# Optimization experiments

Measured on AMD Instinct MI355X. Metric: run time of the kernel, lower is better.

Reference implementation:

```python
import jax, jax.numpy as jnp
import numpy as np

GENES = 20000   # input gene nodes (depth 0)
LEVEL = 10000   # nodes per subsequent depth level
STEPS = 7       # depth propagation steps
DEG = 16        # in-degree per dst node
N = GENES + STEPS * LEVEL          # 90000 total nodes
EPS = LEVEL * DEG                  # 160000 edges per step
E = STEPS * EPS                    # 1120000 total edges
B = 256
C = 2


def setup_inputs() -> dict:
    key = jax.random.key(0)
    k0, k1, k2 = jax.random.split(key, 3)
    X = jax.random.normal(k0, (B, GENES), jnp.float32)
    gene_map = jnp.arange(GENES, dtype=jnp.int32)

    rng = np.random.default_rng(0)
    src_list, dstu_list = [], []
    for k in range(STEPS):
        lo = 0 if k == 0 else GENES + (k - 1) * LEVEL
        hi = GENES if k == 0 else lo + LEVEL
        src_list.append(rng.integers(lo, hi, size=EPS))
        dstu_list.append(np.arange(GENES + k * LEVEL, GENES + (k + 1) * LEVEL))
    src = jnp.asarray(np.stack(src_list), dtype=jnp.int32)          # [STEPS, EPS]
    dst_unique = jnp.asarray(np.stack(dstu_list), dtype=jnp.int32)  # [STEPS, LEVEL]
    dst_pos = jnp.tile(jnp.repeat(jnp.arange(LEVEL, dtype=jnp.int32), DEG)[None, :], (STEPS, 1))
    eid = jnp.arange(E, dtype=jnp.int32).reshape(STEPS, EPS)
    root_ids = dst_unique[-1]

    edge_weight = jax.random.normal(k1, (E,), jnp.float32) * 0.01
    node_bias = jnp.zeros((N,), jnp.float32)
    head_W = jax.random.normal(k2, (LEVEL, C), jnp.float32) * (1.0 / np.sqrt(LEVEL))
    head_b = jnp.zeros((C,), jnp.float32)

    return dict(X=X, edge_weight=edge_weight, node_bias=node_bias,
                head_W=head_W, head_b=head_b, gene_map=gene_map,
                src=src, dst_pos=dst_pos, dst_unique=dst_unique,
                eid=eid, root_ids=root_ids)


def reference(X, edge_weight, node_bias, head_W, head_b,
              gene_map, src, dst_pos, dst_unique, eid, root_ids):
    # dropout is identity (eval mode / p=0)
    b = X.shape[0]
    h = jnp.zeros((b, N), X.dtype).at[:, gene_map].set(X)
    for k in range(src.shape[0]):  # fixed small number of depth steps
        w = edge_weight[eid[k]]                                   # [EPS]
        msg = h[:, src[k]] * w[None, :]                           # gather + scale [B, EPS]
        agg = jnp.zeros((b, dst_unique.shape[1]), h.dtype).at[:, dst_pos[k]].add(msg)
        h_dst = jnp.tanh(agg + node_bias[dst_unique[k]][None, :])  # [B, LEVEL]
        h = h.at[:, dst_unique[k]].set(h_dst)
    roots = h[:, root_ids]                                        # [B, LEVEL]
    return roots @ head_W + head_b
```

## Files before the change

### kernel.cpp

```cpp
#include <hip/hip_runtime.h>
#include <math.h>

#define GENES 20000
#define LEVEL 10000
#define STEPS 7
#define DEG   16
#define EPSZ  (LEVEL * DEG)
#define CCOLS 32
#define NCHUNK 8
#define DBLK  313
#define NGT   625
#define MSTRIDE 18
#define SCOLS 8
#define DPG   1250

typedef unsigned short bf8 __attribute__((ext_vector_type(8)));

__device__ inline float bf2f(unsigned short u) {
    union { unsigned u; float f; } c; c.u = ((unsigned)u) << 16; return c.f;
}
__device__ inline unsigned short f2bf(float x) {
    union { float f; unsigned u; } c; c.f = x;
    return (unsigned short)((c.u + 0x7fffu + ((c.u >> 16) & 1u)) >> 16);
}

__global__ __launch_bounds__(256) void transpose_k(const float* __restrict__ X,
                                                   const int*   __restrict__ gene_map,
                                                   unsigned short* __restrict__ XT) {
    __shared__ float tile[32][33];
    const int chunk = blockIdx.x;
    const int l4  = threadIdx.x & 7;
    const int r8  = threadIdx.x >> 3;
    const int lo  = threadIdx.x & 31;
    const int gr8 = threadIdx.x >> 5;
    unsigned short* XTp = XT + (size_t)chunk * GENES * CCOLS;
    for (int i = 0; i < 4; ++i) {
        const int gt = blockIdx.y * 4 + i;
        if (gt >= NGT) break;
        const int g0 = gt * 32;
        if (i) __syncthreads();
        const float4 xv = *reinterpret_cast<const float4*>(
            X + (size_t)(chunk * CCOLS + r8) * GENES + g0 + l4 * 4);
        tile[r8][l4 * 4 + 0] = xv.x;
        tile[r8][l4 * 4 + 1] = xv.y;
        tile[r8][l4 * 4 + 2] = xv.z;
        tile[r8][l4 * 4 + 3] = xv.w;
        __syncthreads();
#pragma unroll
        for (int jj = 0; jj < 4; ++jj) {
            const int gr   = gr8 + jj * 8;
            const int node = gene_map[g0 + gr];
            XTp[(size_t)node * CCOLS + lo] = f2bf(tile[lo][gr]);
        }
    }
}

__global__ __launch_bounds__(256) void step1_k(const unsigned short* __restrict__ hprev,
                                               unsigned short*       __restrict__ hcur,
                                               const int*   __restrict__ src_k,
                                               const float* __restrict__ w_k,
                                               const float* __restrict__ node_bias,
                                               const int*   __restrict__ dstu_k) {
    const int bid   = blockIdx.x;
    const int chunk = bid & 7;
    const int cb    = bid >> 3;
    const int tid   = threadIdx.x;

    __shared__ int   s_src[32 * MSTRIDE];
    __shared__ float s_w  [32 * MSTRIDE];

    if (tid < 128) {
        const int m4 = cb * 128 + tid;
        if (m4 < EPSZ / 4) {
            const int4 sv = reinterpret_cast<const int4*>(src_k)[m4];
            const int j = tid >> 2, i = (tid & 3) * 4;
            *reinterpret_cast<int4*>(&s_src[j * MSTRIDE + i]) = sv;
        }
    } else {
        const int t  = tid - 128;
        const int m4 = cb * 128 + t;
        if (m4 < EPSZ / 4) {
            const float4 wv = reinterpret_cast<const float4*>(w_k)[m4];
            const int j = t >> 2, i = (t & 3) * 4;
            *reinterpret_cast<float4*>(&s_w[j * MSTRIDE + i]) = wv;
        }
    }
    __syncthreads();

    const int wave = tid >> 6, lane = tid & 63;
    const int c2 = lane & 3;
    const int eh = (lane >> 2) & 1;
    const int q  = lane >> 3;
    const int j  = wave * 8 + q;
    const int dest = cb * 32 + j;
    const int c8 = c2 * 8;

    if (dest < LEVEL) {
        const unsigned short* prev = hprev + (size_t)chunk * GENES * CCOLS;

        const int mb = j * MSTRIDE + eh * 8;
        const int4   sA = *reinterpret_cast<const int4*>  (&s_src[mb]);
        const int4   sB = *reinterpret_cast<const int4*>  (&s_src[mb + 4]);
        const float4 wA = *reinterpret_cast<const float4*>(&s_w  [mb]);
        const float4 wB = *reinterpret_cast<const float4*>(&s_w  [mb + 4]);

#define GL(sv) (*reinterpret_cast<const bf8*>(prev + (size_t)(sv) * CCOLS + c8))
        const bf8 v0 = GL(sA.x);
        const bf8 v1 = GL(sA.y);
        const bf8 v2 = GL(sA.z);
        const bf8 v3 = GL(sA.w);
        const bf8 v4 = GL(sB.x);
        const bf8 v5 = GL(sB.y);
        const bf8 v6 = GL(sB.z);
        const bf8 v7 = GL(sB.w);
#undef GL
        float a0 = 0.f, a1 = 0.f, a2 = 0.f, a3 = 0.f, a4 = 0.f, a5 = 0.f, a6 = 0.f, a7 = 0.f;
#define FMA8(v, wv) { a0 = fmaf(bf2f((v)[0]), (wv), a0); a1 = fmaf(bf2f((v)[1]), (wv), a1);  \
                      a2 = fmaf(bf2f((v)[2]), (wv), a2); a3 = fmaf(bf2f((v)[3]), (wv), a3);  \
                      a4 = fmaf(bf2f((v)[4]), (wv), a4); a5 = fmaf(bf2f((v)[5]), (wv), a5);  \
                      a6 = fmaf(bf2f((v)[6]), (wv), a6); a7 = fmaf(bf2f((v)[7]), (wv), a7); }
        FMA8(v0, wA.x) FMA8(v1, wA.y) FMA8(v2, wA.z) FMA8(v3, wA.w)
        FMA8(v4, wB.x) FMA8(v5, wB.y) FMA8(v6, wB.z) FMA8(v7, wB.w)
#undef FMA8
        a0 += __shfl_xor(a0, 4); a1 += __shfl_xor(a1, 4);
        a2 += __shfl_xor(a2, 4); a3 += __shfl_xor(a3, 4);
        a4 += __shfl_xor(a4, 4); a5 += __shfl_xor(a5, 4);
        a6 += __shfl_xor(a6, 4); a7 += __shfl_xor(a7, 4);

        if (eh == 0) {
            const float bz = node_bias[dstu_k[dest]];
            bf8 o;
            o[0] = f2bf(tanhf(a0 + bz));
            o[1] = f2bf(tanhf(a1 + bz));
            o[2] = f2bf(tanhf(a2 + bz));
            o[3] = f2bf(tanhf(a3 + bz));
            o[4] = f2bf(tanhf(a4 + bz));
            o[5] = f2bf(tanhf(a5 + bz));
            o[6] = f2bf(tanhf(a6 + bz));
            o[7] = f2bf(tanhf(a7 + bz));
            *reinterpret_cast<bf8*>(hcur + ((size_t)(chunk * 4 + c2) * LEVEL + dest) * SCOLS) = o;
        }
    }
}

__global__ __launch_bounds__(1024) void sstep_k(
        const unsigned short* __restrict__ hprev,
        unsigned short*       __restrict__ hcur,
        const int*   __restrict__ src_k,
        const float* __restrict__ w_k,
        const float* __restrict__ node_bias,
        const int*   __restrict__ dstu_k,
        int src_base) {
    __shared__ unsigned short slice[LEVEL * SCOLS];
    const int bid = blockIdx.x;
    const int cc  = (bid & 7) * 4 + ((bid >> 3) & 3);
    const int g   = bid >> 5;
    const int tid = threadIdx.x;

    const int d0 = g * DPG + tid;
    const int be0 = d0 * DEG;
    const int4   sA = *reinterpret_cast<const int4*>  (src_k + be0);
    const int4   sB = *reinterpret_cast<const int4*>  (src_k + be0 + 4);
    const int4   sC = *reinterpret_cast<const int4*>  (src_k + be0 + 8);
    const int4   sD = *reinterpret_cast<const int4*>  (src_k + be0 + 12);
    const float4 wA = *reinterpret_cast<const float4*>(w_k + be0);
    const float4 wB = *reinterpret_cast<const float4*>(w_k + be0 + 4);
    const float4 wC = *reinterpret_cast<const float4*>(w_k + be0 + 8);
    const float4 wD = *reinterpret_cast<const float4*>(w_k + be0 + 12);

    const unsigned short* pc = hprev + (size_t)cc * LEVEL * SCOLS;
#pragma unroll
    for (int i = 0; i < 10; ++i) {
        const int row = i * 1024 + tid;
        if (row < LEVEL)
            *reinterpret_cast<bf8*>(&slice[row * SCOLS]) =
                *reinterpret_cast<const bf8*>(pc + (size_t)row * SCOLS);
    }
    __syncthreads();

    unsigned short* oc = hcur + (size_t)cc * LEVEL * SCOLS;

#define ACC(sv, wv) { const int row = (sv) - src_base;                                      \
    const bf8 v = *reinterpret_cast<const bf8*>(&slice[row * SCOLS]);                       \
    a0 = fmaf(bf2f(v[0]), (wv), a0); a1 = fmaf(bf2f(v[1]), (wv), a1);                       \
    a2 = fmaf(bf2f(v[2]), (wv), a2); a3 = fmaf(bf2f(v[3]), (wv), a3);                       \
    a4 = fmaf(bf2f(v[4]), (wv), a4); a5 = fmaf(bf2f(v[5]), (wv), a5);                       \
    a6 = fmaf(bf2f(v[6]), (wv), a6); a7 = fmaf(bf2f(v[7]), (wv), a7); }

    {
        float a0 = 0.f, a1 = 0.f, a2 = 0.f, a3 = 0.f, a4 = 0.f, a5 = 0.f, a6 = 0.f, a7 = 0.f;
        ACC(sA.x, wA.x) ACC(sA.y, wA.y) ACC(sA.z, wA.z) ACC(sA.w, wA.w)
        ACC(sB.x, wB.x) ACC(sB.y, wB.y) ACC(sB.z, wB.z) ACC(sB.w, wB.w)
        ACC(sC.x, wC.x) ACC(sC.y, wC.y) ACC(sC.z, wC.z) ACC(sC.w, wC.w)
        ACC(sD.x, wD.x) ACC(sD.y, wD.y) ACC(sD.z, wD.z) ACC(sD.w, wD.w)
        const float bz = node_bias[dstu_k[d0]];
        bf8 o;
        o[0] = f2bf(tanhf(a0 + bz));
        o[1] = f2bf(tanhf(a1 + bz));
        o[2] = f2bf(tanhf(a2 + bz));
        o[3] = f2bf(tanhf(a3 + bz));
        o[4] = f2bf(tanhf(a4 + bz));
        o[5] = f2bf(tanhf(a5 + bz));
        o[6] = f2bf(tanhf(a6 + bz));
        o[7] = f2bf(tanhf(a7 + bz));
        *reinterpret_cast<bf8*>(oc + (size_t)d0 * SCOLS) = o;
    }

    if (tid < DPG - 1024) {
        const int d1 = g * DPG + 1024 + tid;
        const int be1 = d1 * DEG;
        const int4   tA = *reinterpret_cast<const int4*>  (src_k + be1);
        const int4   tB = *reinterpret_cast<const int4*>  (src_k + be1 + 4);
        const int4   tC = *reinterpret_cast<const int4*>  (src_k + be1 + 8);
        const int4   tD = *reinterpret_cast<const int4*>  (src_k + be1 + 12);
        const float4 uA = *reinterpret_cast<const float4*>(w_k + be1);
        const float4 uB = *reinterpret_cast<const float4*>(w_k + be1 + 4);
        const float4 uC = *reinterpret_cast<const float4*>(w_k + be1 + 8);
        const float4 uD = *reinterpret_cast<const float4*>(w_k + be1 + 12);
        float a0 = 0.f, a1 = 0.f, a2 = 0.f, a3 = 0.f, a4 = 0.f, a5 = 0.f, a6 = 0.f, a7 = 0.f;
        ACC(tA.x, uA.x) ACC(tA.y, uA.y) ACC(tA.z, uA.z) ACC(tA.w, uA.w)
        ACC(tB.x, uB.x) ACC(tB.y, uB.y) ACC(tB.z, uB.z) ACC(tB.w, uB.w)
        ACC(tC.x, uC.x) ACC(tC.y, uC.y) ACC(tC.z, uC.z) ACC(tC.w, uC.w)
        ACC(tD.x, uD.x) ACC(tD.y, uD.y) ACC(tD.z, uD.z) ACC(tD.w, uD.w)
        const float bz = node_bias[dstu_k[d1]];
        bf8 o;
        o[0] = f2bf(tanhf(a0 + bz));
        o[1] = f2bf(tanhf(a1 + bz));
        o[2] = f2bf(tanhf(a2 + bz));
        o[3] = f2bf(tanhf(a3 + bz));
        o[4] = f2bf(tanhf(a4 + bz));
        o[5] = f2bf(tanhf(a5 + bz));
        o[6] = f2bf(tanhf(a6 + bz));
        o[7] = f2bf(tanhf(a7 + bz));
        *reinterpret_cast<bf8*>(oc + (size_t)d1 * SCOLS) = o;
    }
#undef ACC
}

__global__ __launch_bounds__(1024) void sstep7_k(
        const unsigned short* __restrict__ hprev,
        const int*   __restrict__ src_k,
        const float* __restrict__ w_k,
        const float* __restrict__ node_bias,
        const int*   __restrict__ dstu_k,
        const float* __restrict__ head_W,
        float*       __restrict__ part,
        int src_base) {
    __shared__ unsigned short slice[LEVEL * SCOLS];
    __shared__ float red[16][16];
    const int bid = blockIdx.x;
    const int cc  = (bid & 7) * 4 + ((bid >> 3) & 3);
    const int g   = bid >> 5;
    const int tid = threadIdx.x;

    const int d0 = g * DPG + tid;
    const int be0 = d0 * DEG;
    const int4   sA = *reinterpret_cast<const int4*>  (src_k + be0);
    const int4   sB = *reinterpret_cast<const int4*>  (src_k + be0 + 4);
    const int4   sC = *reinterpret_cast<const int4*>  (src_k + be0 + 8);
    const int4   sD = *reinterpret_cast<const int4*>  (src_k + be0 + 12);
    const float4 wA = *reinterpret_cast<const float4*>(w_k + be0);
    const float4 wB = *reinterpret_cast<const float4*>(w_k + be0 + 4);
    const float4 wC = *reinterpret_cast<const float4*>(w_k + be0 + 8);
    const float4 wD = *reinterpret_cast<const float4*>(w_k + be0 + 12);

    const unsigned short* pc = hprev + (size_t)cc * LEVEL * SCOLS;
#pragma unroll
    for (int i = 0; i < 10; ++i) {
        const int row = i * 1024 + tid;
        if (row < LEVEL)
            *reinterpret_cast<bf8*>(&slice[row * SCOLS]) =
                *reinterpret_cast<const bf8*>(pc + (size_t)row * SCOLS);
    }
    __syncthreads();

    float h[16];
#pragma unroll
    for (int v = 0; v < 16; ++v) h[v] = 0.f;

#define ACC(sv, wv) { const int row = (sv) - src_base;                                      \
    const bf8 v = *reinterpret_cast<const bf8*>(&slice[row * SCOLS]);                       \
    a0 = fmaf(bf2f(v[0]), (wv), a0); a1 = fmaf(bf2f(v[1]), (wv), a1);                       \
    a2 = fmaf(bf2f(v[2]), (wv), a2); a3 = fmaf(bf2f(v[3]), (wv), a3);                       \
    a4 = fmaf(bf2f(v[4]), (wv), a4); a5 = fmaf(bf2f(v[5]), (wv), a5);                       \
    a6 = fmaf(bf2f(v[6]), (wv), a6); a7 = fmaf(bf2f(v[7]), (wv), a7); }
#define HEADU(d) {                                                                           \
        const float bz = node_bias[dstu_k[d]];                                               \
        const float o0 = tanhf(a0 + bz), o1 = tanhf(a1 + bz);                                \
        const float o2 = tanhf(a2 + bz), o3 = tanhf(a3 + bz);                                \
        const float o4 = tanhf(a4 + bz), o5 = tanhf(a5 + bz);                                \
        const float o6 = tanhf(a6 + bz), o7 = tanhf(a7 + bz);                                \
        const float2 wv = *reinterpret_cast<const float2*>(head_W + (size_t)(d) * 2);        \
        h[0]  = fmaf(o0, wv.x, h[0]);  h[1]  = fmaf(o0, wv.y, h[1]);                         \
        h[2]  = fmaf(o1, wv.x, h[2]);  h[3]  = fmaf(o1, wv.y, h[3]);                         \
        h[4]  = fmaf(o2, wv.x, h[4]);  h[5]  = fmaf(o2, wv.y, h[5]);                         \
        h[6]  = fmaf(o3, wv.x, h[6]);  h[7]  = fmaf(o3, wv.y, h[7]);                         \
        h[8]  = fmaf(o4, wv.x, h[8]);  h[9]  = fmaf(o4, wv.y, h[9]);                         \
        h[10] = fmaf(o5, wv.x, h[10]); h[11] = fmaf(o5, wv.y, h[11]);                        \
        h[12] = fmaf(o6, wv.x, h[12]); h[13] = fmaf(o6, wv.y, h[13]);                        \
        h[14] = fmaf(o7, wv.x, h[14]); h[15] = fmaf(o7, wv.y, h[15]); }

    {
        float a0 = 0.f, a1 = 0.f, a2 = 0.f, a3 = 0.f, a4 = 0.f, a5 = 0.f, a6 = 0.f, a7 = 0.f;
        ACC(sA.x, wA.x) ACC(sA.y, wA.y) ACC(sA.z, wA.z) ACC(sA.w, wA.w)
        ACC(sB.x, wB.x) ACC(sB.y, wB.y) ACC(sB.z, wB.z) ACC(sB.w, wB.w)
        ACC(sC.x, wC.x) ACC(sC.y, wC.y) ACC(sC.z, wC.z) ACC(sC.w, wC.w)
        ACC(sD.x, wD.x) ACC(sD.y, wD.y) ACC(sD.z, wD.z) ACC(sD.w, wD.w)
        HEADU(d0)
    }
    if (tid < DPG - 1024) {
        const int d1 = g * DPG + 1024 + tid;
        const int be1 = d1 * DEG;
        const int4   tA = *reinterpret_cast<const int4*>  (src_k + be1);
        const int4   tB = *reinterpret_cast<const int4*>  (src_k + be1 + 4);
        const int4   tC = *reinterpret_cast<const int4*>  (src_k + be1 + 8);
        const int4   tD = *reinterpret_cast<const int4*>  (src_k + be1 + 12);
        const float4 uA = *reinterpret_cast<const float4*>(w_k + be1);
        const float4 uB = *reinterpret_cast<const float4*>(w_k + be1 + 4);
        const float4 uC = *reinterpret_cast<const float4*>(w_k + be1 + 8);
        const float4 uD = *reinterpret_cast<const float4*>(w_k + be1 + 12);
        float a0 = 0.f, a1 = 0.f, a2 = 0.f, a3 = 0.f, a4 = 0.f, a5 = 0.f, a6 = 0.f, a7 = 0.f;
        ACC(tA.x, uA.x) ACC(tA.y, uA.y) ACC(tA.z, uA.z) ACC(tA.w, uA.w)
        ACC(tB.x, uB.x) ACC(tB.y, uB.y) ACC(tB.z, uB.z) ACC(tB.w, uB.w)
        ACC(tC.x, uC.x) ACC(tC.y, uC.y) ACC(tC.z, uC.z) ACC(tC.w, uC.w)
        ACC(tD.x, uD.x) ACC(tD.y, uD.y) ACC(tD.z, uD.z) ACC(tD.w, uD.w)
        HEADU(d1)
    }
#undef HEADU
#undef ACC

    const int wave = tid >> 6, lane = tid & 63;
#pragma unroll
    for (int m = 1; m < 64; m <<= 1) {
#pragma unroll
        for (int v = 0; v < 16; ++v) h[v] += __shfl_xor(h[v], m);
    }
    if (lane == 0) {
#pragma unroll
        for (int v = 0; v < 16; ++v) red[wave][v] = h[v];
    }
    __syncthreads();
    if (tid < 16) {
        float s = 0.f;
#pragma unroll
        for (int w = 0; w < 16; ++w) s += red[w][tid];
        part[((size_t)cc * 8 + g) * 16 + tid] = s;
    }
}

__global__ __launch_bounds__(512) void head_final_k(const float* __restrict__ part,
                                                    const float* __restrict__ head_b,
                                                    float*       __restrict__ out) {
    const int tid = threadIdx.x;
    const int cc = tid >> 4, v = tid & 15;
    float acc = head_b[v & 1];
#pragma unroll
    for (int g = 0; g < 8; ++g)
        acc += part[((size_t)cc * 8 + g) * 16 + v];
    const int b = (cc >> 2) * 32 + (cc & 3) * 8 + (v >> 1);
    out[b * 2 + (v & 1)] = acc;
}

extern "C" void kernel_launch(void* const* d_in, const int* in_sizes, int n_in,
                              void* d_out, int out_size, void* d_ws, size_t ws_size,
                              hipStream_t stream) {
    const float* X           = (const float*)d_in[0];
    const float* edge_weight = (const float*)d_in[1];
    const float* node_bias   = (const float*)d_in[2];
    const float* head_W      = (const float*)d_in[3];
    const float* head_b      = (const float*)d_in[4];
    const int*   gene_map    = (const int*)  d_in[5];
    const int*   src         = (const int*)  d_in[6];
    const int*   dst_unique  = (const int*)  d_in[8];
    float* out = (float*)d_out;

    char* ws = (char*)d_ws;
    unsigned short* XT   = (unsigned short*)(ws);
    unsigned short* lvlA = (unsigned short*)(ws + 10240000);
    unsigned short* lvlB = (unsigned short*)(ws + 15360000);
    float*          part = (float*)         (ws + 20480000);

    transpose_k<<<dim3(NCHUNK, 157), 256, 0, stream>>>(X, gene_map, XT);

    step1_k<<<DBLK * NCHUNK, 256, 0, stream>>>(XT, lvlA, src, edge_weight,
                                               node_bias, dst_unique);

    unsigned short* bufs[2] = {lvlA, lvlB};
    for (int k = 1; k <= 5; ++k) {
        sstep_k<<<256, 1024, 0, stream>>>(bufs[(k - 1) & 1], bufs[k & 1],
                                          src + (size_t)k * EPSZ,
                                          edge_weight + (size_t)k * EPSZ,
                                          node_bias,
                                          dst_unique + (size_t)k * LEVEL,
                                          GENES + (k - 1) * LEVEL);
    }

    sstep7_k<<<256, 1024, 0, stream>>>(bufs[1],
                                       src + (size_t)6 * EPSZ,
                                       edge_weight + (size_t)6 * EPSZ,
                                       node_bias,
                                       dst_unique + (size_t)6 * LEVEL,
                                       head_W, part,
                                       GENES + 5 * LEVEL);
    head_final_k<<<1, 512, 0, stream>>>(part, head_b, out);
    (void)in_sizes; (void)n_in; (void)out_size; (void)ws_size;
}
```

Baseline: 79.22 us.

## Fuse depth steps 2-7 and head into one persistent kernel with per-chunk counters

Replaces the six per-step launches plus the final head-reduction kernel with one persistent kernel of 256 blocks. Blocks that share a column chunk synchronise through atomic counters in global memory, and each level is written to its own buffer. The weight and index loads for the next step are issued before the wait, so they overlap it. The aim is to remove launch gaps and the tail of each kernel, at the cost of spin-waiting. The design also relies on all 256 blocks being co-resident, and it adds a memset launch.

Result: slower. 138.4 us (+74.7%).

```diff
diff --git a/kernel.cpp b/kernel.cpp
--- a/kernel.cpp
+++ b/kernel.cpp
@@ -3,7 +3,6 @@
 
 #define GENES 20000
 #define LEVEL 10000
-#define STEPS 7
 #define DEG   16
 #define EPSZ  (LEVEL * DEG)
 #define CCOLS 32
@@ -13,6 +12,7 @@
 #define MSTRIDE 18
 #define SCOLS 8
 #define DPG   1250
+#define LVLSZ ((size_t)32 * LEVEL * SCOLS)
 
 typedef unsigned short bf8 __attribute__((ext_vector_type(8)));
 
@@ -143,149 +143,36 @@
     }
 }
 
-__global__ __launch_bounds__(1024) void sstep_k(
-        const unsigned short* __restrict__ hprev,
-        unsigned short*       __restrict__ hcur,
-        const int*   __restrict__ src_k,
-        const float* __restrict__ w_k,
+__global__ __launch_bounds__(1024, 1) void fused_k(
+        unsigned short* lvl,
+        const int*   __restrict__ src,
+        const float* __restrict__ ew,
         const float* __restrict__ node_bias,
-        const int*   __restrict__ dstu_k,
-        int src_base) {
-    __shared__ unsigned short slice[LEVEL * SCOLS];
-    const int bid = blockIdx.x;
-    const int cc  = (bid & 7) * 4 + ((bid >> 3) & 3);
-    const int g   = bid >> 5;
-    const int tid = threadIdx.x;
-
-    const int d0 = g * DPG + tid;
-    const int be0 = d0 * DEG;
-    const int4   sA = *reinterpret_cast<const int4*>  (src_k + be0);
-    const int4   sB = *reinterpret_cast<const int4*>  (src_k + be0 + 4);
-    const int4   sC = *reinterpret_cast<const int4*>  (src_k + be0 + 8);
-    const int4   sD = *reinterpret_cast<const int4*>  (src_k + be0 + 12);
-    const float4 wA = *reinterpret_cast<const float4*>(w_k + be0);
-    const float4 wB = *reinterpret_cast<const float4*>(w_k + be0 + 4);
-    const float4 wC = *reinterpret_cast<const float4*>(w_k + be0 + 8);
-    const float4 wD = *reinterpret_cast<const float4*>(w_k + be0 + 12);
-
-    const unsigned short* pc = hprev + (size_t)cc * LEVEL * SCOLS;
-#pragma unroll
-    for (int i = 0; i < 10; ++i) {
-        const int row = i * 1024 + tid;
-        if (row < LEVEL)
-            *reinterpret_cast<bf8*>(&slice[row * SCOLS]) =
-                *reinterpret_cast<const bf8*>(pc + (size_t)row * SCOLS);
-    }
-    __syncthreads();
-
-    unsigned short* oc = hcur + (size_t)cc * LEVEL * SCOLS;
-
-#define ACC(sv, wv) { const int row = (sv) - src_base;                                      \
-    const bf8 v = *reinterpret_cast<const bf8*>(&slice[row * SCOLS]);                       \
-    a0 = fmaf(bf2f(v[0]), (wv), a0); a1 = fmaf(bf2f(v[1]), (wv), a1);                       \
-    a2 = fmaf(bf2f(v[2]), (wv), a2); a3 = fmaf(bf2f(v[3]), (wv), a3);                       \
-    a4 = fmaf(bf2f(v[4]), (wv), a4); a5 = fmaf(bf2f(v[5]), (wv), a5);                       \
-    a6 = fmaf(bf2f(v[6]), (wv), a6); a7 = fmaf(bf2f(v[7]), (wv), a7); }
-
-    {
-        float a0 = 0.f, a1 = 0.f, a2 = 0.f, a3 = 0.f, a4 = 0.f, a5 = 0.f, a6 = 0.f, a7 = 0.f;
-        ACC(sA.x, wA.x) ACC(sA.y, wA.y) ACC(sA.z, wA.z) ACC(sA.w, wA.w)
-        ACC(sB.x, wB.x) ACC(sB.y, wB.y) ACC(sB.z, wB.z) ACC(sB.w, wB.w)
-        ACC(sC.x, wC.x) ACC(sC.y, wC.y) ACC(sC.z, wC.z) ACC(sC.w, wC.w)
-        ACC(sD.x, wD.x) ACC(sD.y, wD.y) ACC(sD.z, wD.z) ACC(sD.w, wD.w)
-        const float bz = node_bias[dstu_k[d0]];
-        bf8 o;
-        o[0] = f2bf(tanhf(a0 + bz));
-        o[1] = f2bf(tanhf(a1 + bz));
-        o[2] = f2bf(tanhf(a2 + bz));
-        o[3] = f2bf(tanhf(a3 + bz));
-        o[4] = f2bf(tanhf(a4 + bz));
-        o[5] = f2bf(tanhf(a5 + bz));
-        o[6] = f2bf(tanhf(a6 + bz));
-        o[7] = f2bf(tanhf(a7 + bz));
-        *reinterpret_cast<bf8*>(oc + (size_t)d0 * SCOLS) = o;
-    }
-
-    if (tid < DPG - 1024) {
-        const int d1 = g * DPG + 1024 + tid;
-        const int be1 = d1 * DEG;
-        const int4   tA = *reinterpret_cast<const int4*>  (src_k + be1);
-        const int4   tB = *reinterpret_cast<const int4*>  (src_k + be1 + 4);
-        const int4   tC = *reinterpret_cast<const int4*>  (src_k + be1 + 8);
-        const int4   tD = *reinterpret_cast<const int4*>  (src_k + be1 + 12);
-        const float4 uA = *reinterpret_cast<const float4*>(w_k + be1);
-        const float4 uB = *reinterpret_cast<const float4*>(w_k + be1 + 4);
-        const float4 uC = *reinterpret_cast<const float4*>(w_k + be1 + 8);
-        const float4 uD = *reinterpret_cast<const float4*>(w_k + be1 + 12);
-        float a0 = 0.f, a1 = 0.f, a2 = 0.f, a3 = 0.f, a4 = 0.f, a5 = 0.f, a6 = 0.f, a7 = 0.f;
-        ACC(tA.x, uA.x) ACC(tA.y, uA.y) ACC(tA.z, uA.z) ACC(tA.w, uA.w)
-        ACC(tB.x, uB.x) ACC(tB.y, uB.y) ACC(tB.z, uB.z) ACC(tB.w, uB.w)
-        ACC(tC.x, uC.x) ACC(tC.y, uC.y) ACC(tC.z, uC.z) ACC(tC.w, uC.w)
-        ACC(tD.x, uD.x) ACC(tD.y, uD.y) ACC(tD.z, uD.z) ACC(tD.w, uD.w)
-        const float bz = node_bias[dstu_k[d1]];
-        bf8 o;
-        o[0] = f2bf(tanhf(a0 + bz));
-        o[1] = f2bf(tanhf(a1 + bz));
-        o[2] = f2bf(tanhf(a2 + bz));
-        o[3] = f2bf(tanhf(a3 + bz));
-        o[4] = f2bf(tanhf(a4 + bz));
-        o[5] = f2bf(tanhf(a5 + bz));
-        o[6] = f2bf(tanhf(a6 + bz));
-        o[7] = f2bf(tanhf(a7 + bz));
-        *reinterpret_cast<bf8*>(oc + (size_t)d1 * SCOLS) = o;
-    }
-#undef ACC
-}
-
-__global__ __launch_bounds__(1024) void sstep7_k(
-        const unsigned short* __restrict__ hprev,
-        const int*   __restrict__ src_k,
-        const float* __restrict__ w_k,
-        const float* __restrict__ node_bias,
-        const int*   __restrict__ dstu_k,
+        const int*   __restrict__ dst_unique,
         const float* __restrict__ head_W,
-        float*       __restrict__ part,
-        int src_base) {
+        const float* __restrict__ head_b,
+        float* __restrict__ part,
+        int*   __restrict__ cnt,
+        float* __restrict__ out) {
     __shared__ unsigned short slice[LEVEL * SCOLS];
     __shared__ float red[16][16];
     const int bid = blockIdx.x;
     const int cc  = (bid & 7) * 4 + ((bid >> 3) & 3);
     const int g   = bid >> 5;
     const int tid = threadIdx.x;
-
-    const int d0 = g * DPG + tid;
+    int* cc_cnt = cnt + cc * 16;
+
+    const int d0  = g * DPG + tid;
     const int be0 = d0 * DEG;
-    const int4   sA = *reinterpret_cast<const int4*>  (src_k + be0);
-    const int4   sB = *reinterpret_cast<const int4*>  (src_k + be0 + 4);
-    const int4   sC = *reinterpret_cast<const int4*>  (src_k + be0 + 8);
-    const int4   sD = *reinterpret_cast<const int4*>  (src_k + be0 + 12);
-    const float4 wA = *reinterpret_cast<const float4*>(w_k + be0);
-    const float4 wB = *reinterpret_cast<const float4*>(w_k + be0 + 4);
-    const float4 wC = *reinterpret_cast<const float4*>(w_k + be0 + 8);
-    const float4 wD = *reinterpret_cast<const float4*>(w_k + be0 + 12);
-
-    const unsigned short* pc = hprev + (size_t)cc * LEVEL * SCOLS;
-#pragma unroll
-    for (int i = 0; i < 10; ++i) {
-        const int row = i * 1024 + tid;
-        if (row < LEVEL)
-            *reinterpret_cast<bf8*>(&slice[row * SCOLS]) =
-                *reinterpret_cast<const bf8*>(pc + (size_t)row * SCOLS);
-    }
-    __syncthreads();
-
-    float h[16];
-#pragma unroll
-    for (int v = 0; v < 16; ++v) h[v] = 0.f;
-
-#define ACC(sv, wv) { const int row = (sv) - src_base;                                      \
+
+#define ACC(sv, wv) { const int row = (sv) - base;                                          \
     const bf8 v = *reinterpret_cast<const bf8*>(&slice[row * SCOLS]);                       \
     a0 = fmaf(bf2f(v[0]), (wv), a0); a1 = fmaf(bf2f(v[1]), (wv), a1);                       \
     a2 = fmaf(bf2f(v[2]), (wv), a2); a3 = fmaf(bf2f(v[3]), (wv), a3);                       \
     a4 = fmaf(bf2f(v[4]), (wv), a4); a5 = fmaf(bf2f(v[5]), (wv), a5);                       \
     a6 = fmaf(bf2f(v[6]), (wv), a6); a7 = fmaf(bf2f(v[7]), (wv), a7); }
 #define HEADU(d) {                                                                           \
-        const float bz = node_bias[dstu_k[d]];                                               \
+        const float bz = node_bias[dstu[d]];                                                 \
         const float o0 = tanhf(a0 + bz), o1 = tanhf(a1 + bz);                                \
         const float o2 = tanhf(a2 + bz), o3 = tanhf(a3 + bz);                                \
         const float o4 = tanhf(a4 + bz), o5 = tanhf(a5 + bz);                                \
@@ -300,65 +187,156 @@
         h[12] = fmaf(o6, wv.x, h[12]); h[13] = fmaf(o6, wv.y, h[13]);                        \
         h[14] = fmaf(o7, wv.x, h[14]); h[15] = fmaf(o7, wv.y, h[15]); }
 
-    {
-        float a0 = 0.f, a1 = 0.f, a2 = 0.f, a3 = 0.f, a4 = 0.f, a5 = 0.f, a6 = 0.f, a7 = 0.f;
-        ACC(sA.x, wA.x) ACC(sA.y, wA.y) ACC(sA.z, wA.z) ACC(sA.w, wA.w)
-        ACC(sB.x, wB.x) ACC(sB.y, wB.y) ACC(sB.z, wB.z) ACC(sB.w, wB.w)
-        ACC(sC.x, wC.x) ACC(sC.y, wC.y) ACC(sC.z, wC.z) ACC(sC.w, wC.w)
-        ACC(sD.x, wD.x) ACC(sD.y, wD.y) ACC(sD.z, wD.z) ACC(sD.w, wD.w)
-        HEADU(d0)
-    }
-    if (tid < DPG - 1024) {
-        const int d1 = g * DPG + 1024 + tid;
-        const int be1 = d1 * DEG;
-        const int4   tA = *reinterpret_cast<const int4*>  (src_k + be1);
-        const int4   tB = *reinterpret_cast<const int4*>  (src_k + be1 + 4);
-        const int4   tC = *reinterpret_cast<const int4*>  (src_k + be1 + 8);
-        const int4   tD = *reinterpret_cast<const int4*>  (src_k + be1 + 12);
-        const float4 uA = *reinterpret_cast<const float4*>(w_k + be1);
-        const float4 uB = *reinterpret_cast<const float4*>(w_k + be1 + 4);
-        const float4 uC = *reinterpret_cast<const float4*>(w_k + be1 + 8);
-        const float4 uD = *reinterpret_cast<const float4*>(w_k + be1 + 12);
-        float a0 = 0.f, a1 = 0.f, a2 = 0.f, a3 = 0.f, a4 = 0.f, a5 = 0.f, a6 = 0.f, a7 = 0.f;
-        ACC(tA.x, uA.x) ACC(tA.y, uA.y) ACC(tA.z, uA.z) ACC(tA.w, uA.w)
-        ACC(tB.x, uB.x) ACC(tB.y, uB.y) ACC(tB.z, uB.z) ACC(tB.w, uB.w)
-        ACC(tC.x, uC.x) ACC(tC.y, uC.y) ACC(tC.z, uC.z) ACC(tC.w, uC.w)
-        ACC(tD.x, uD.x) ACC(tD.y, uD.y) ACC(tD.z, uD.z) ACC(tD.w, uD.w)
-        HEADU(d1)
+    for (int s = 0; s < 6; ++s) {
+        const int*   srck = src + (size_t)(s + 1) * EPSZ;
+        const float* wk   = ew  + (size_t)(s + 1) * EPSZ;
+        const int*   dstu = dst_unique + (size_t)(s + 1) * LEVEL;
+        const int    base = GENES + s * LEVEL;
+
+        const int4   sA = *reinterpret_cast<const int4*>  (srck + be0);
+        const int4   sB = *reinterpret_cast<const int4*>  (srck + be0 + 4);
+        const int4   sC = *reinterpret_cast<const int4*>  (srck + be0 + 8);
+        const int4   sD = *reinterpret_cast<const int4*>  (srck + be0 + 12);
+        const float4 wA = *reinterpret_cast<const float4*>(wk + be0);
+        const float4 wB = *reinterpret_cast<const float4*>(wk + be0 + 4);
+        const float4 wC = *reinterpret_cast<const float4*>(wk + be0 + 8);
+        const float4 wD = *reinterpret_cast<const float4*>(wk + be0 + 12);
+
+        if (s > 0 && tid == 0) {
+            while (__hip_atomic_load(cc_cnt, __ATOMIC_RELAXED, __HIP_MEMORY_SCOPE_AGENT) < 8 * s)
+                __builtin_amdgcn_s_sleep(1);
+        }
+        __syncthreads();
+
+        const unsigned short* pc = lvl + (size_t)s * LVLSZ + (size_t)cc * LEVEL * SCOLS;
+#pragma unroll
+        for (int i = 0; i < 10; ++i) {
+            const int row = i * 1024 + tid;
+            if (row < LEVEL)
+                *reinterpret_cast<bf8*>(&slice[row * SCOLS]) =
+                    *reinterpret_cast<const bf8*>(pc + (size_t)row * SCOLS);
+        }
+        __syncthreads();
+
+        if (s < 5) {
+            unsigned short* oc = lvl + (size_t)(s + 1) * LVLSZ + (size_t)cc * LEVEL * SCOLS;
+            {
+                float a0 = 0.f, a1 = 0.f, a2 = 0.f, a3 = 0.f, a4 = 0.f, a5 = 0.f, a6 = 0.f, a7 = 0.f;
+                ACC(sA.x, wA.x) ACC(sA.y, wA.y) ACC(sA.z, wA.z) ACC(sA.w, wA.w)
+                ACC(sB.x, wB.x) ACC(sB.y, wB.y) ACC(sB.z, wB.z) ACC(sB.w, wB.w)
+                ACC(sC.x, wC.x) ACC(sC.y, wC.y) ACC(sC.z, wC.z) ACC(sC.w, wC.w)
+                ACC(sD.x, wD.x) ACC(sD.y, wD.y) ACC(sD.z, wD.z) ACC(sD.w, wD.w)
+                const float bz = node_bias[dstu[d0]];
+                bf8 o;
+                o[0] = f2bf(tanhf(a0 + bz));
+                o[1] = f2bf(tanhf(a1 + bz));
+                o[2] = f2bf(tanhf(a2 + bz));
+                o[3] = f2bf(tanhf(a3 + bz));
+                o[4] = f2bf(tanhf(a4 + bz));
+                o[5] = f2bf(tanhf(a5 + bz));
+                o[6] = f2bf(tanhf(a6 + bz));
+                o[7] = f2bf(tanhf(a7 + bz));
+                *reinterpret_cast<bf8*>(oc + (size_t)d0 * SCOLS) = o;
+            }
+            if (tid < DPG - 1024) {
+                const int d1 = g * DPG + 1024 + tid;
+                const int be1 = d1 * DEG;
+                const int4   tA = *reinterpret_cast<const int4*>  (srck + be1);
+                const int4   tB = *reinterpret_cast<const int4*>  (srck + be1 + 4);
+                const int4   tC = *reinterpret_cast<const int4*>  (srck + be1 + 8);
+                const int4   tD = *reinterpret_cast<const int4*>  (srck + be1 + 12);
+                const float4 uA = *reinterpret_cast<const float4*>(wk + be1);
+                const float4 uB = *reinterpret_cast<const float4*>(wk + be1 + 4);
+                const float4 uC = *reinterpret_cast<const float4*>(wk + be1 + 8);
+                const float4 uD = *reinterpret_cast<const float4*>(wk + be1 + 12);
+                float a0 = 0.f, a1 = 0.f, a2 = 0.f, a3 = 0.f, a4 = 0.f, a5 = 0.f, a6 = 0.f, a7 = 0.f;
+                ACC(tA.x, uA.x) ACC(tA.y, uA.y) ACC(tA.z, uA.z) ACC(tA.w, uA.w)
+                ACC(tB.x, uB.x) ACC(tB.y, uB.y) ACC(tB.z, uB.z) ACC(tB.w, uB.w)
+                ACC(tC.x, uC.x) ACC(tC.y, uC.y) ACC(tC.z, uC.z) ACC(tC.w, uC.w)
+                ACC(tD.x, uD.x) ACC(tD.y, uD.y) ACC(tD.z, uD.z) ACC(tD.w, uD.w)
+                const float bz = node_bias[dstu[d1]];
+                bf8 o;
+                o[0] = f2bf(tanhf(a0 + bz));
+                o[1] = f2bf(tanhf(a1 + bz));
+                o[2] = f2bf(tanhf(a2 + bz));
+                o[3] = f2bf(tanhf(a3 + bz));
+                o[4] = f2bf(tanhf(a4 + bz));
+                o[5] = f2bf(tanhf(a5 + bz));
+                o[6] = f2bf(tanhf(a6 + bz));
+                o[7] = f2bf(tanhf(a7 + bz));
+                *reinterpret_cast<bf8*>(oc + (size_t)d1 * SCOLS) = o;
+            }
+        } else {
+            float h[16];
+#pragma unroll
+            for (int v = 0; v < 16; ++v) h[v] = 0.f;
+            {
+                float a0 = 0.f, a1 = 0.f, a2 = 0.f, a3 = 0.f, a4 = 0.f, a5 = 0.f, a6 = 0.f, a7 = 0.f;
+                ACC(sA.x, wA.x) ACC(sA.y, wA.y) ACC(sA.z, wA.z) ACC(sA.w, wA.w)
+                ACC(sB.x, wB.x) ACC(sB.y, wB.y) ACC(sB.z, wB.z) ACC(sB.w, wB.w)
+                ACC(sC.x, wC.x) ACC(sC.y, wC.y) ACC(sC.z, wC.z) ACC(sC.w, wC.w)
+                ACC(sD.x, wD.x) ACC(sD.y, wD.y) ACC(sD.z, wD.z) ACC(sD.w, wD.w)
+                HEADU(d0)
+            }
+            if (tid < DPG - 1024) {
+                const int d1 = g * DPG + 1024 + tid;
+                const int be1 = d1 * DEG;
+                const int4   tA = *reinterpret_cast<const int4*>  (srck + be1);
+                const int4   tB = *reinterpret_cast<const int4*>  (srck + be1 + 4);
+                const int4   tC = *reinterpret_cast<const int4*>  (srck + be1 + 8);
+                const int4   tD = *reinterpret_cast<const int4*>  (srck + be1 + 12);
+                const float4 uA = *reinterpret_cast<const float4*>(wk + be1);
+                const float4 uB = *reinterpret_cast<const float4*>(wk + be1 + 4);
+                const float4 uC = *reinterpret_cast<const float4*>(wk + be1 + 8);
+                const float4 uD = *reinterpret_cast<const float4*>(wk + be1 + 12);
+                float a0 = 0.f, a1 = 0.f, a2 = 0.f, a3 = 0.f, a4 = 0.f, a5 = 0.f, a6 = 0.f, a7 = 0.f;
+                ACC(tA.x, uA.x) ACC(tA.y, uA.y) ACC(tA.z, uA.z) ACC(tA.w, uA.w)
+                ACC(tB.x, uB.x) ACC(tB.y, uB.y) ACC(tB.z, uB.z) ACC(tB.w, uB.w)
+                ACC(tC.x, uC.x) ACC(tC.y, uC.y) ACC(tC.z, uC.z) ACC(tC.w, uC.w)
+                ACC(tD.x, uD.x) ACC(tD.y, uD.y) ACC(tD.z, uD.z) ACC(tD.w, uD.w)
+                HEADU(d1)
+            }
+            const int wave = tid >> 6, lane = tid & 63;
+#pragma unroll
+            for (int m = 1; m < 64; m <<= 1) {
+#pragma unroll
+                for (int v = 0; v < 16; ++v) h[v] += __shfl_xor(h[v], m);
+            }
+            if (lane == 0) {
+#pragma unroll
+                for (int v = 0; v < 16; ++v) red[wave][v] = h[v];
+            }
+            __syncthreads();
+            if (tid < 16) {
+                float sum = 0.f;
+#pragma unroll
+                for (int w = 0; w < 16; ++w) sum += red[w][tid];
+                part[((size_t)cc * 8 + g) * 16 + tid] = sum;
+            }
+        }
+
+        __syncthreads();
+        if (tid == 0)
+            __hip_atomic_fetch_add(cc_cnt, 1, __ATOMIC_RELEASE, __HIP_MEMORY_SCOPE_AGENT);
     }
 #undef HEADU
 #undef ACC
 
-    const int wave = tid >> 6, lane = tid & 63;
-#pragma unroll
-    for (int m = 1; m < 64; m <<= 1) {
-#pragma unroll
-        for (int v = 0; v < 16; ++v) h[v] += __shfl_xor(h[v], m);
-    }
-    if (lane == 0) {
-#pragma unroll
-        for (int v = 0; v < 16; ++v) red[wave][v] = h[v];
-    }
-    __syncthreads();
-    if (tid < 16) {
-        float s = 0.f;
-#pragma unroll
-        for (int w = 0; w < 16; ++w) s += red[w][tid];
-        part[((size_t)cc * 8 + g) * 16 + tid] = s;
-    }
-}
-
-__global__ __launch_bounds__(512) void head_final_k(const float* __restrict__ part,
-                                                    const float* __restrict__ head_b,
-                                                    float*       __restrict__ out) {
-    const int tid = threadIdx.x;
-    const int cc = tid >> 4, v = tid & 15;
-    float acc = head_b[v & 1];
-#pragma unroll
-    for (int g = 0; g < 8; ++g)
-        acc += part[((size_t)cc * 8 + g) * 16 + v];
-    const int b = (cc >> 2) * 32 + (cc & 3) * 8 + (v >> 1);
-    out[b * 2 + (v & 1)] = acc;
+    if (g == 0) {
+        if (tid == 0) {
+            while (__hip_atomic_load(cc_cnt, __ATOMIC_RELAXED, __HIP_MEMORY_SCOPE_AGENT) < 48)
+                __builtin_amdgcn_s_sleep(1);
+        }
+        __syncthreads();
+        if (tid < 16) {
+            float acc = head_b[tid & 1];
+#pragma unroll
+            for (int q = 0; q < 8; ++q)
+                acc += part[((size_t)cc * 8 + q) * 16 + tid];
+            const int b = (cc >> 2) * 32 + (cc & 3) * 8 + (tid >> 1);
+            out[b * 2 + (tid & 1)] = acc;
+        }
+    }
 }
 
 extern "C" void kernel_launch(void* const* d_in, const int* in_sizes, int n_in,
@@ -376,32 +354,18 @@
 
     char* ws = (char*)d_ws;
     unsigned short* XT   = (unsigned short*)(ws);
-    unsigned short* lvlA = (unsigned short*)(ws + 10240000);
-    unsigned short* lvlB = (unsigned short*)(ws + 15360000);
-    float*          part = (float*)         (ws + 20480000);
+    unsigned short* lvl  = (unsigned short*)(ws + 10240000);
+    float*          part = (float*)         (ws + 40960000);
+    int*            cnt  = (int*)           (ws + 40976384);
+
+    hipMemsetAsync(cnt, 0, 32 * 16 * sizeof(int), stream);
 
     transpose_k<<<dim3(NCHUNK, 157), 256, 0, stream>>>(X, gene_map, XT);
 
-    step1_k<<<DBLK * NCHUNK, 256, 0, stream>>>(XT, lvlA, src, edge_weight,
+    step1_k<<<DBLK * NCHUNK, 256, 0, stream>>>(XT, lvl, src, edge_weight,
                                                node_bias, dst_unique);
 
-    unsigned short* bufs[2] = {lvlA, lvlB};
-    for (int k = 1; k <= 5; ++k) {
-        sstep_k<<<256, 1024, 0, stream>>>(bufs[(k - 1) & 1], bufs[k & 1],
-                                          src + (size_t)k * EPSZ,
-                                          edge_weight + (size_t)k * EPSZ,
-                                          node_bias,
-                                          dst_unique + (size_t)k * LEVEL,
-                                          GENES + (k - 1) * LEVEL);
-    }
-
-    sstep7_k<<<256, 1024, 0, stream>>>(bufs[1],
-                                       src + (size_t)6 * EPSZ,
-                                       edge_weight + (size_t)6 * EPSZ,
-                                       node_bias,
-                                       dst_unique + (size_t)6 * LEVEL,
-                                       head_W, part,
-                                       GENES + 5 * LEVEL);
-    head_final_k<<<1, 512, 0, stream>>>(part, head_b, out);
+    fused_k<<<256, 1024, 0, stream>>>(lvl, src, edge_weight, node_bias,
+                                      dst_unique, head_W, head_b, part, cnt, out);
     (void)in_sizes; (void)n_in; (void)out_size; (void)ws_size;
 }
```

## Stage gene-level slices in LDS for step one, matching later step kernels

Applied to the files above, without the earlier changes.

The transposed input is now laid out as 32 column-groups of 8 batch columns. The first propagation step is replaced by a 1024-thread kernel that loads the 20000 gene rows into shared memory in two 10000-row passes and accumulates only the edges whose source falls in each pass. This mirrors the layout and shared-memory gather scheme of the later steps and replaces scattered global gathers with LDS reads. The cost is two passes with a barrier between them, a bounds check on every edge, and only 256 blocks, each processing 1250 destinations with large LDS use.

Measured after the change: 86.12 us. 1.09x slower.

```diff
diff --git a/kernel.cpp b/kernel.cpp
--- a/kernel.cpp
+++ b/kernel.cpp
@@ -3,14 +3,9 @@
 
 #define GENES 20000
 #define LEVEL 10000
-#define STEPS 7
 #define DEG   16
 #define EPSZ  (LEVEL * DEG)
-#define CCOLS 32
-#define NCHUNK 8
-#define DBLK  313
 #define NGT   625
-#define MSTRIDE 18
 #define SCOLS 8
 #define DPG   1250
 
@@ -28,19 +23,20 @@
                                                    const int*   __restrict__ gene_map,
                                                    unsigned short* __restrict__ XT) {
     __shared__ float tile[32][33];
-    const int chunk = blockIdx.x;
+    const int bt  = blockIdx.x;
     const int l4  = threadIdx.x & 7;
     const int r8  = threadIdx.x >> 3;
     const int lo  = threadIdx.x & 31;
     const int gr8 = threadIdx.x >> 5;
-    unsigned short* XTp = XT + (size_t)chunk * GENES * CCOLS;
+    const int cc  = bt * 4 + (lo >> 3);
+    const int cw  = lo & 7;
     for (int i = 0; i < 4; ++i) {
         const int gt = blockIdx.y * 4 + i;
         if (gt >= NGT) break;
         const int g0 = gt * 32;
         if (i) __syncthreads();
         const float4 xv = *reinterpret_cast<const float4*>(
-            X + (size_t)(chunk * CCOLS + r8) * GENES + g0 + l4 * 4);
+            X + (size_t)(bt * 32 + r8) * GENES + g0 + l4 * 4);
         tile[r8][l4 * 4 + 0] = xv.x;
         tile[r8][l4 * 4 + 1] = xv.y;
         tile[r8][l4 * 4 + 2] = xv.z;
@@ -50,96 +46,124 @@
         for (int jj = 0; jj < 4; ++jj) {
             const int gr   = gr8 + jj * 8;
             const int node = gene_map[g0 + gr];
-            XTp[(size_t)node * CCOLS + lo] = f2bf(tile[lo][gr]);
+            XT[((size_t)cc * GENES + node) * SCOLS + cw] = f2bf(tile[lo][gr]);
         }
     }
 }
 
-__global__ __launch_bounds__(256) void step1_k(const unsigned short* __restrict__ hprev,
-                                               unsigned short*       __restrict__ hcur,
-                                               const int*   __restrict__ src_k,
-                                               const float* __restrict__ w_k,
-                                               const float* __restrict__ node_bias,
-                                               const int*   __restrict__ dstu_k) {
-    const int bid   = blockIdx.x;
-    const int chunk = bid & 7;
-    const int cb    = bid >> 3;
-    const int tid   = threadIdx.x;
-
-    __shared__ int   s_src[32 * MSTRIDE];
-    __shared__ float s_w  [32 * MSTRIDE];
-
-    if (tid < 128) {
-        const int m4 = cb * 128 + tid;
-        if (m4 < EPSZ / 4) {
-            const int4 sv = reinterpret_cast<const int4*>(src_k)[m4];
-            const int j = tid >> 2, i = (tid & 3) * 4;
-            *reinterpret_cast<int4*>(&s_src[j * MSTRIDE + i]) = sv;
+__global__ __launch_bounds__(1024) void step1s_k(
+        const unsigned short* __restrict__ XT,
+        unsigned short*       __restrict__ hcur,
+        const int*   __restrict__ src_k,
+        const float* __restrict__ w_k,
+        const float* __restrict__ node_bias,
+        const int*   __restrict__ dstu_k) {
+    __shared__ unsigned short slice[LEVEL * SCOLS];
+    const int bid = blockIdx.x;
+    const int cc  = (bid & 7) * 4 + ((bid >> 3) & 3);
+    const int g   = bid >> 5;
+    const int tid = threadIdx.x;
+
+    const int d0  = g * DPG + tid;
+    const int be0 = d0 * DEG;
+    const int4   sA = *reinterpret_cast<const int4*>  (src_k + be0);
+    const int4   sB = *reinterpret_cast<const int4*>  (src_k + be0 + 4);
+    const int4   sC = *reinterpret_cast<const int4*>  (src_k + be0 + 8);
+    const int4   sD = *reinterpret_cast<const int4*>  (src_k + be0 + 12);
+    const float4 wA = *reinterpret_cast<const float4*>(w_k + be0);
+    const float4 wB = *reinterpret_cast<const float4*>(w_k + be0 + 4);
+    const float4 wC = *reinterpret_cast<const float4*>(w_k + be0 + 8);
+    const float4 wD = *reinterpret_cast<const float4*>(w_k + be0 + 12);
+
+    const bool valid1 = (tid < DPG - 1024);
+    const int d1  = g * DPG + 1024 + tid;
+    int4 tA = {0,0,0,0}, tB = {0,0,0,0}, tC = {0,0,0,0}, tD = {0,0,0,0};
+    float4 uA = {0,0,0,0}, uB = {0,0,0,0}, uC = {0,0,0,0}, uD = {0,0,0,0};
+    if (valid1) {
+        const int be1 = d1 * DEG;
+        tA = *reinterpret_cast<const int4*>  (src_k + be1);
+        tB = *reinterpret_cast<const int4*>  (src_k + be1 + 4);
+        tC = *reinterpret_cast<const int4*>  (src_k + be1 + 8);
+        tD = *reinterpret_cast<const int4*>  (src_k + be1 + 12);
+        uA = *reinterpret_cast<const float4*>(w_k + d1 * DEG);
+        uB = *reinterpret_cast<const float4*>(w_k + d1 * DEG + 4);
+        uC = *reinterpret_cast<const float4*>(w_k + d1 * DEG + 8);
+        uD = *reinterpret_cast<const float4*>(w_k + d1 * DEG + 12);
+    }
+
+    float a0 = 0.f, a1 = 0.f, a2 = 0.f, a3 = 0.f, a4 = 0.f, a5 = 0.f, a6 = 0.f, a7 = 0.f;
+    float b0 = 0.f, b1 = 0.f, b2 = 0.f, b3 = 0.f, b4 = 0.f, b5 = 0.f, b6 = 0.f, b7 = 0.f;
+
+    const unsigned short* xc = XT + (size_t)cc * GENES * SCOLS;
+
+#define ACCP(acc0,acc1,acc2,acc3,acc4,acc5,acc6,acc7, sv, wv) {                              \
+    const int row = (sv) - pbase;                                                            \
+    if ((unsigned)row < (unsigned)LEVEL) {                                                   \
+        const bf8 v = *reinterpret_cast<const bf8*>(&slice[row * SCOLS]);                    \
+        acc0 = fmaf(bf2f(v[0]), (wv), acc0); acc1 = fmaf(bf2f(v[1]), (wv), acc1);            \
+        acc2 = fmaf(bf2f(v[2]), (wv), acc2); acc3 = fmaf(bf2f(v[3]), (wv), acc3);            \
+        acc4 = fmaf(bf2f(v[4]), (wv), acc4); acc5 = fmaf(bf2f(v[5]), (wv), acc5);            \
+        acc6 = fmaf(bf2f(v[6]), (wv), acc6); acc7 = fmaf(bf2f(v[7]), (wv), acc7); } }
+
+    for (int p = 0; p < 2; ++p) {
+        const int pbase = p * LEVEL;
+        if (p) __syncthreads();
+#pragma unroll
+        for (int i = 0; i < 10; ++i) {
+            const int row = i * 1024 + tid;
+            if (row < LEVEL)
+                *reinterpret_cast<bf8*>(&slice[row * SCOLS]) =
+                    *reinterpret_cast<const bf8*>(xc + (size_t)(pbase + row) * SCOLS);
         }
-    } else {
-        const int t  = tid - 128;
-        const int m4 = cb * 128 + t;
-        if (m4 < EPSZ / 4) {
-            const float4 wv = reinterpret_cast<const float4*>(w_k)[m4];
-            const int j = t >> 2, i = (t & 3) * 4;
-            *reinterpret_cast<float4*>(&s_w[j * MSTRIDE + i]) = wv;
+        __syncthreads();
+
+        ACCP(a0,a1,a2,a3,a4,a5,a6,a7, sA.x, wA.x) ACCP(a0,a1,a2,a3,a4,a5,a6,a7, sA.y, wA.y)
+        ACCP(a0,a1,a2,a3,a4,a5,a6,a7, sA.z, wA.z) ACCP(a0,a1,a2,a3,a4,a5,a6,a7, sA.w, wA.w)
+        ACCP(a0,a1,a2,a3,a4,a5,a6,a7, sB.x, wB.x) ACCP(a0,a1,a2,a3,a4,a5,a6,a7, sB.y, wB.y)
+        ACCP(a0,a1,a2,a3,a4,a5,a6,a7, sB.z, wB.z) ACCP(a0,a1,a2,a3,a4,a5,a6,a7, sB.w, wB.w)
+        ACCP(a0,a1,a2,a3,a4,a5,a6,a7, sC.x, wC.x) ACCP(a0,a1,a2,a3,a4,a5,a6,a7, sC.y, wC.y)
+        ACCP(a0,a1,a2,a3,a4,a5,a6,a7, sC.z, wC.z) ACCP(a0,a1,a2,a3,a4,a5,a6,a7, sC.w, wC.w)
+        ACCP(a0,a1,a2,a3,a4,a5,a6,a7, sD.x, wD.x) ACCP(a0,a1,a2,a3,a4,a5,a6,a7, sD.y, wD.y)
+        ACCP(a0,a1,a2,a3,a4,a5,a6,a7, sD.z, wD.z) ACCP(a0,a1,a2,a3,a4,a5,a6,a7, sD.w, wD.w)
+        if (valid1) {
+            ACCP(b0,b1,b2,b3,b4,b5,b6,b7, tA.x, uA.x) ACCP(b0,b1,b2,b3,b4,b5,b6,b7, tA.y, uA.y)
+            ACCP(b0,b1,b2,b3,b4,b5,b6,b7, tA.z, uA.z) ACCP(b0,b1,b2,b3,b4,b5,b6,b7, tA.w, uA.w)
+            ACCP(b0,b1,b2,b3,b4,b5,b6,b7, tB.x, uB.x) ACCP(b0,b1,b2,b3,b4,b5,b6,b7, tB.y, uB.y)
+            ACCP(b0,b1,b2,b3,b4,b5,b6,b7, tB.z, uB.z) ACCP(b0,b1,b2,b3,b4,b5,b6,b7, tB.w, uB.w)
+            ACCP(b0,b1,b2,b3,b4,b5,b6,b7, tC.x, uC.x) ACCP(b0,b1,b2,b3,b4,b5,b6,b7, tC.y, uC.y)
+            ACCP(b0,b1,b2,b3,b4,b5,b6,b7, tC.z, uC.z) ACCP(b0,b1,b2,b3,b4,b5,b6,b7, tC.w, uC.w)
+            ACCP(b0,b1,b2,b3,b4,b5,b6,b7, tD.x, uD.x) ACCP(b0,b1,b2,b3,b4,b5,b6,b7, tD.y, uD.y)
+            ACCP(b0,b1,b2,b3,b4,b5,b6,b7, tD.z, uD.z) ACCP(b0,b1,b2,b3,b4,b5,b6,b7, tD.w, uD.w)
         }
     }
-    __syncthreads();
-
-    const int wave = tid >> 6, lane = tid & 63;
-    const int c2 = lane & 3;
-    const int eh = (lane >> 2) & 1;
-    const int q  = lane >> 3;
-    const int j  = wave * 8 + q;
-    const int dest = cb * 32 + j;
-    const int c8 = c2 * 8;
-
-    if (dest < LEVEL) {
-        const unsigned short* prev = hprev + (size_t)chunk * GENES * CCOLS;
-
-        const int mb = j * MSTRIDE + eh * 8;
-        const int4   sA = *reinterpret_cast<const int4*>  (&s_src[mb]);
-        const int4   sB = *reinterpret_cast<const int4*>  (&s_src[mb + 4]);
-        const float4 wA = *reinterpret_cast<const float4*>(&s_w  [mb]);
-        const float4 wB = *reinterpret_cast<const float4*>(&s_w  [mb + 4]);
-
-#define GL(sv) (*reinterpret_cast<const bf8*>(prev + (size_t)(sv) * CCOLS + c8))
-        const bf8 v0 = GL(sA.x);
-        const bf8 v1 = GL(sA.y);
-        const bf8 v2 = GL(sA.z);
-        const bf8 v3 = GL(sA.w);
-        const bf8 v4 = GL(sB.x);
-        const bf8 v5 = GL(sB.y);
-        const bf8 v6 = GL(sB.z);
-        const bf8 v7 = GL(sB.w);
-#undef GL
-        float a0 = 0.f, a1 = 0.f, a2 = 0.f, a3 = 0.f, a4 = 0.f, a5 = 0.f, a6 = 0.f, a7 = 0.f;
-#define FMA8(v, wv) { a0 = fmaf(bf2f((v)[0]), (wv), a0); a1 = fmaf(bf2f((v)[1]), (wv), a1);  \
-                      a2 = fmaf(bf2f((v)[2]), (wv), a2); a3 = fmaf(bf2f((v)[3]), (wv), a3);  \
-                      a4 = fmaf(bf2f((v)[4]), (wv), a4); a5 = fmaf(bf2f((v)[5]), (wv), a5);  \
-                      a6 = fmaf(bf2f((v)[6]), (wv), a6); a7 = fmaf(bf2f((v)[7]), (wv), a7); }
-        FMA8(v0, wA.x) FMA8(v1, wA.y) FMA8(v2, wA.z) FMA8(v3, wA.w)
-        FMA8(v4, wB.x) FMA8(v5, wB.y) FMA8(v6, wB.z) FMA8(v7, wB.w)
-#undef FMA8
-        a0 += __shfl_xor(a0, 4); a1 += __shfl_xor(a1, 4);
-        a2 += __shfl_xor(a2, 4); a3 += __shfl_xor(a3, 4);
-        a4 += __shfl_xor(a4, 4); a5 += __shfl_xor(a5, 4);
-        a6 += __shfl_xor(a6, 4); a7 += __shfl_xor(a7, 4);
-
-        if (eh == 0) {
-            const float bz = node_bias[dstu_k[dest]];
-            bf8 o;
-            o[0] = f2bf(tanhf(a0 + bz));
-            o[1] = f2bf(tanhf(a1 + bz));
-            o[2] = f2bf(tanhf(a2 + bz));
-            o[3] = f2bf(tanhf(a3 + bz));
-            o[4] = f2bf(tanhf(a4 + bz));
-            o[5] = f2bf(tanhf(a5 + bz));
-            o[6] = f2bf(tanhf(a6 + bz));
-            o[7] = f2bf(tanhf(a7 + bz));
-            *reinterpret_cast<bf8*>(hcur + ((size_t)(chunk * 4 + c2) * LEVEL + dest) * SCOLS) = o;
-        }
+#undef ACCP
+
+    unsigned short* oc = hcur + (size_t)cc * LEVEL * SCOLS;
+    {
+        const float bz = node_bias[dstu_k[d0]];
+        bf8 o;
+        o[0] = f2bf(tanhf(a0 + bz));
+        o[1] = f2bf(tanhf(a1 + bz));
+        o[2] = f2bf(tanhf(a2 + bz));
+        o[3] = f2bf(tanhf(a3 + bz));
+        o[4] = f2bf(tanhf(a4 + bz));
+        o[5] = f2bf(tanhf(a5 + bz));
+        o[6] = f2bf(tanhf(a6 + bz));
+        o[7] = f2bf(tanhf(a7 + bz));
+        *reinterpret_cast<bf8*>(oc + (size_t)d0 * SCOLS) = o;
+    }
+    if (valid1) {
+        const float bz = node_bias[dstu_k[d1]];
+        bf8 o;
+        o[0] = f2bf(tanhf(b0 + bz));
+        o[1] = f2bf(tanhf(b1 + bz));
+        o[2] = f2bf(tanhf(b2 + bz));
+        o[3] = f2bf(tanhf(b3 + bz));
+        o[4] = f2bf(tanhf(b4 + bz));
+        o[5] = f2bf(tanhf(b5 + bz));
+        o[6] = f2bf(tanhf(b6 + bz));
+        o[7] = f2bf(tanhf(b7 + bz));
+        *reinterpret_cast<bf8*>(oc + (size_t)d1 * SCOLS) = o;
     }
 }
 
@@ -380,10 +404,10 @@
     unsigned short* lvlB = (unsigned short*)(ws + 15360000);
     float*          part = (float*)         (ws + 20480000);
 
-    transpose_k<<<dim3(NCHUNK, 157), 256, 0, stream>>>(X, gene_map, XT);
-
-    step1_k<<<DBLK * NCHUNK, 256, 0, stream>>>(XT, lvlA, src, edge_weight,
-                                               node_bias, dst_unique);
+    transpose_k<<<dim3(8, 157), 256, 0, stream>>>(X, gene_map, XT);
+
+    step1s_k<<<256, 1024, 0, stream>>>(XT, lvlA, src, edge_weight,
+                                       node_bias, dst_unique);
 
     unsigned short* bufs[2] = {lvlA, lvlB};
     for (int k = 1; k <= 5; ++k) {
```
